# Optimization experiments

Hardware: AMD Instinct MI355X
Metric: run time of the kernel (lower is better)

The kernel has to match this reference:

```python
import jax, jax.numpy as jnp
import numpy as np

HID = 4096; H = 32; KVH = 8; D = 128
B = 4; Q = 256; KV = 2048; HIST = KV - Q
BS = 64; NB = KV // BS; NBLOCKS = 160
WINDOW = 1024; THETA = 10000.0


def _rope(x, pos):
    # x: [T, heads, D], pos: [T] absolute positions
    half = D // 2
    inv = 1.0 / (THETA ** (jnp.arange(half, dtype=jnp.float32) / half))
    f = pos.astype(jnp.float32)[:, None] * inv[None, :]          # [T, D/2]
    cos = jnp.concatenate([jnp.cos(f), jnp.cos(f)], -1)[:, None, :]
    sin = jnp.concatenate([jnp.sin(f), jnp.sin(f)], -1)[:, None, :]
    x1, x2 = jnp.split(x, 2, axis=-1)
    return x * cos + jnp.concatenate([-x2, x1], -1) * sin


def setup_inputs() -> dict:
    key = jax.random.key(0)
    ks = jax.random.split(key, 7)
    T = B * Q
    return dict(
        hidden_states=jax.random.normal(ks[0], (T, HID), jnp.float32),
        wq=jax.random.normal(ks[1], (HID, H * D), jnp.float32) * 0.02,
        wk=jax.random.normal(ks[2], (HID, KVH * D), jnp.float32) * 0.02,
        wv=jax.random.normal(ks[3], (HID, KVH * D), jnp.float32) * 0.02,
        wo=jax.random.normal(ks[4], (H * D, HID), jnp.float32) * 0.02,
        k_cache=jax.random.normal(ks[5], (NBLOCKS, BS, KVH, D), jnp.float32),
        v_cache=jax.random.normal(ks[6], (NBLOCKS, BS, KVH, D), jnp.float32),
        # each sequence appends Q new tokens at positions [HIST, KV)
        position_ids=jnp.tile(HIST + jnp.arange(Q, dtype=jnp.int32), B),
        q_start_loc=jnp.arange(B, dtype=jnp.int32) * Q,
        q_seq_length=jnp.full((B,), Q, jnp.int32),
        kv_seq_length=jnp.full((B,), KV, jnp.int32),
        block_offsets=jnp.arange(B * NB, dtype=jnp.int32).reshape(B, NB),
    )


def reference(hidden_states, wq, wk, wv, wo, k_cache, v_cache,
              position_ids, q_start_loc, q_seq_length, kv_seq_length,
              block_offsets):
    # qkv proj (no bias, Mistral)
    q = (hidden_states @ wq).reshape(-1, H, D)    # [T, H, D]
    k = (hidden_states @ wk).reshape(-1, KVH, D)  # [T, KVH, D]
    v = (hidden_states @ wv).reshape(-1, KVH, D)
    # rotary embedding on q, k with per-token absolute positions
    q = _rope(q, position_ids)
    k = _rope(k, position_ids)
    # fill paged KV cache: token with in-sequence slot s of sequence b goes to
    # block block_offsets[b, s // BS], offset s % BS
    b_idx = jnp.repeat(jnp.arange(B), Q)
    blk = block_offsets[b_idx, position_ids // BS]
    off = position_ids % BS
    k_cache = k_cache.at[blk, off].set(k)
    v_cache = v_cache.at[blk, off].set(v)
    # paged attention: gather each sequence's blocks from the cache
    k_all = k_cache[block_offsets].reshape(B, KV, KVH, D)
    v_all = v_cache[block_offsets].reshape(B, KV, KVH, D)
    G = H // KVH  # GQA group size
    qb = q.reshape(B, Q, KVH, G, D)
    scores = jnp.einsum('bqhgd,bkhd->bhgqk', qb, k_all) / jnp.sqrt(jnp.float32(D))
    # causal + sliding-window mask on absolute positions
    qpos = HIST + jnp.arange(Q)
    kpos = jnp.arange(KV)
    valid = (kpos[None, :] <= qpos[:, None]) & (kpos[None, :] > qpos[:, None] - WINDOW)
    scores = jnp.where(valid[None, None, None], scores, -jnp.inf)
    p = jax.nn.softmax(scores, axis=-1)
    o = jnp.einsum('bhgqk,bkhd->bqhgd', p, v_all).reshape(B * Q, H * D)
    return o @ wo
```

## Files before the change

kernel.cpp:

```cpp
#include <hip/hip_runtime.h>

#define BSZ  4
#define QL   256
#define KVL  2048
#define HIST 1792
#define WIN  1024
#define NH   32
#define NKVH 8
#define DH   128
#define HID  4096
#define SCALE 0.088388347648318447f
#define MFIX  8.0f

typedef __bf16 bf16x8 __attribute__((ext_vector_type(8)));
typedef float  fx4    __attribute__((ext_vector_type(4)));
typedef unsigned short us4 __attribute__((ext_vector_type(4)));
typedef unsigned short us8 __attribute__((ext_vector_type(8)));

__device__ __forceinline__ unsigned short f2bf(float x) {
    unsigned u = __float_as_uint(x);
    u += 0x7FFFu + ((u >> 16) & 1u);
    return (unsigned short)(u >> 16);
}
__device__ __forceinline__ float bf2f(unsigned short h) {
    return __uint_as_float(((unsigned)h) << 16);
}
__device__ __forceinline__ fx4 mfma16(bf16x8 a, bf16x8 b, fx4 c) {
    return __builtin_amdgcn_mfma_f32_16x16x32_bf16(a, b, c, 0, 0, 0);
}
__device__ __forceinline__ bf16x8 ldb16(const unsigned short* p) {
    return *reinterpret_cast<const bf16x8*>(p);
}

typedef __attribute__((address_space(1))) const void gv_t;
typedef __attribute__((address_space(3))) void lv_t;
__device__ __forceinline__ void gl16(const void* g, void* l) {
    __builtin_amdgcn_global_load_lds((gv_t*)g, (lv_t*)l, 16, 0, 0);
}

__device__ __forceinline__ void gemm_body(
    const unsigned short* __restrict__ A, const unsigned short* __restrict__ B,
    float* __restrict__ C0, float* __restrict__ Cz, size_t czstride,
    int lda, int ldc, int ksteps, int klast, int nx, int ny, int nz)
{
    constexpr int TILE = 128 * 32;
    __shared__ __align__(16) unsigned short lds[3 * 2 * TILE];

    const int per = gridDim.x >> 3;
    const int t = (blockIdx.x & 7) * per + (blockIdx.x >> 3);
    const int bx = t % nx;
    const int by = (t / nx) % ny;
    const int bz = t / (nx * ny);

    const int row0 = bx * 128;
    const int col0 = by * 128;
    const int kbase = bz * ksteps * 32;
    const int nks = (bz == nz - 1) ? klast : ksteps;
    float* Cm = (bz == 0) ? C0 : (Cz + (size_t)(bz - 1) * czstride);

    const int tid  = threadIdx.x;
    const int lane = tid & 63;
    const int w    = tid >> 6;
    const int wr   = w >> 1, wc = w & 1;
    const int l16  = lane & 15;
    const int lg   = lane >> 4;
    const int r_in = lane >> 2;
    const int c8   = (lane & 3) * 8;

    fx4 acc[4][4] = {};

    auto STAGE = [&](int bufi, int kp) {
        unsigned short* Lb = lds + bufi * (2 * TILE);
#pragma unroll
        for (int i = 0; i < 2; ++i) {
            const int r = w * 32 + i * 16 + r_in;
            const int ldsb = (w * 2 + i) * 512;
            gl16(A + (size_t)(row0 + r) * lda + kp + c8, Lb + ldsb);
            const int cr = col0 + r;
            const size_t baddr = ((size_t)(cr >> 6) * 64 + (kp >> 6)) * 4096
                               + (cr & 63) * 64 + (kp & 63) + c8;
            gl16(B + baddr, Lb + TILE + ldsb);
        }
    };

    STAGE(0, kbase);
    STAGE(1, kbase + 32);
    for (int ks = 0; ks < nks; ++ks) {
        if (ks + 2 < nks) {
            STAGE((ks + 2) % 3, kbase + (ks + 2) * 32);
            asm volatile("s_waitcnt vmcnt(8)" ::: "memory");
        } else if (ks + 1 < nks) {
            asm volatile("s_waitcnt vmcnt(4)" ::: "memory");
        } else {
            asm volatile("s_waitcnt vmcnt(0)" ::: "memory");
        }
        __builtin_amdgcn_s_barrier();
        __builtin_amdgcn_sched_barrier(0);

        const unsigned short* Lb = lds + (ks % 3) * (2 * TILE);
        const unsigned short* AhT = Lb;
        const unsigned short* BhT = Lb + TILE;

        bf16x8 af[4], bfv[4];
#pragma unroll
        for (int f = 0; f < 4; ++f) {
            af[f]  = ldb16(AhT + (wr * 64 + f * 16 + l16) * 32 + lg * 8);
            bfv[f] = ldb16(BhT + (wc * 64 + f * 16 + l16) * 32 + lg * 8);
        }
        __builtin_amdgcn_s_setprio(1);
#pragma unroll
        for (int fr = 0; fr < 4; ++fr)
#pragma unroll
            for (int fc = 0; fc < 4; ++fc)
                acc[fr][fc] = mfma16(af[fr], bfv[fc], acc[fr][fc]);
        __builtin_amdgcn_s_setprio(0);
        __builtin_amdgcn_sched_barrier(0);
        __builtin_amdgcn_s_barrier();
    }
#pragma unroll
    for (int fr = 0; fr < 4; ++fr)
#pragma unroll
        for (int fc = 0; fc < 4; ++fc) {
            const size_t rbase = (size_t)(row0 + wr * 64 + fr * 16 + lg * 4);
            const int col = col0 + wc * 64 + fc * 16 + l16;
#pragma unroll
            for (int r = 0; r < 4; ++r)
                Cm[(rbase + r) * ldc + col] = acc[fr][fc][r];
        }
}

__global__ __launch_bounds__(256) void qkv_gemm_kernel(
    const unsigned short* __restrict__ A, const unsigned short* __restrict__ B,
    float* __restrict__ C0, float* __restrict__ Cz, size_t czstride,
    int lda, int ldc, int ksteps, int klast, int nx, int ny, int nz)
{
    gemm_body(A, B, C0, Cz, czstride, lda, ldc, ksteps, klast, nx, ny, nz);
}

__global__ __launch_bounds__(256) void oproj_gemm_kernel(
    const unsigned short* __restrict__ A, const unsigned short* __restrict__ B,
    float* __restrict__ C0, float* __restrict__ Cz, size_t czstride,
    int lda, int ldc, int ksteps, int klast, int nx, int ny, int nz)
{
    gemm_body(A, B, C0, Cz, czstride, lda, ldc, ksteps, klast, nx, ny, nz);
}

__device__ __forceinline__ void transpose_tile(
    const float* __restrict__ w, unsigned short* __restrict__ hi, int N,
    int n0, int k0)
{
    __shared__ __align__(16) float shf[64][64];
    const int tid = threadIdx.x;
    const int rr = tid >> 4;
    const int cc = (tid & 15) * 4;
#pragma unroll
    for (int p = 0; p < 4; ++p) {
        const int kl = p * 16 + rr;
        fx4 v = *reinterpret_cast<const fx4*>(w + (size_t)(k0 + kl) * N + n0 + cc);
#pragma unroll
        for (int j = 0; j < 4; ++j) {
            const int n = cc + j;
            shf[n][kl ^ (n & 28)] = v[j];
        }
    }
    __syncthreads();
    unsigned short* ob = hi + (((size_t)(n0 >> 6)) * 64 + (k0 >> 6)) * 4096;
#pragma unroll
    for (int s = 0; s < 2; ++s) {
        const int c = s * 256 + tid;
        const int n = c >> 3;
        const int k8 = (c & 7) * 8;
        const int sw = n & 28;
        const int b0 = (k8 ^ (sw & 24)) | (sw & 4);
        fx4 v0 = *reinterpret_cast<const fx4*>(&shf[n][b0]);
        fx4 v1 = *reinterpret_cast<const fx4*>(&shf[n][b0 ^ 4]);
        us8 o;
#pragma unroll
        for (int j = 0; j < 4; ++j) {
            o[j]     = f2bf(v0[j]);
            o[4 + j] = f2bf(v1[j]);
        }
        *reinterpret_cast<us8*>(ob + c * 8) = o;
    }
}

__global__ __launch_bounds__(256) void prep_kernel(
    const float* __restrict__ wq, const float* __restrict__ wk,
    const float* __restrict__ wv, const float* __restrict__ wo,
    const float* __restrict__ hs,
    unsigned short* __restrict__ wqkvT, unsigned short* __restrict__ woTh,
    unsigned short* __restrict__ hsb, float* __restrict__ tab)
{
    const int r = blockIdx.x;
    const int tid = threadIdx.x;
    if (r < 4096) {
        transpose_tile(wq, wqkvT, 4096, (r & 63) * 64, (r >> 6) * 64);
    } else if (r < 5120) {
        const int r2 = r - 4096;
        transpose_tile(wk, wqkvT + (size_t)4096 * 4096, 1024,
                       (r2 & 15) * 64, (r2 >> 4) * 64);
    } else if (r < 6144) {
        const int r2 = r - 5120;
        transpose_tile(wv, wqkvT + (size_t)5120 * 4096, 1024,
                       (r2 & 15) * 64, (r2 >> 4) * 64);
    } else if (r < 10240) {
        const int r2 = r - 6144;
        transpose_tile(wo, woTh, 4096, (r2 & 63) * 64, (r2 >> 6) * 64);
    } else if (r < 12288) {
        const int r2 = r - 10240;
        int i = r2 * 256 + tid;
#pragma unroll
        for (int rep = 0; rep < 2; ++rep) {
            fx4 v = reinterpret_cast<const fx4*>(hs)[i];
            us4 o;
#pragma unroll
            for (int j = 0; j < 4; ++j) o[j] = f2bf(v[j]);
            reinterpret_cast<us4*>(hsb)[i] = o;
            i += 524288;
        }
    } else {
        const int r2 = r - 12288;
        const int qi = r2 * 4 + (tid >> 6);
        const int jr = tid & 63;
        const float inv = powf(10000.f, -(float)jr * (1.f / 64.f));
        const float f = (float)(HIST + qi) * inv;
        float s, c;
        sincosf(f, &s, &c);
        tab[(qi * 64 + jr) * 2]     = c;
        tab[(qi * 64 + jr) * 2 + 1] = s;
    }
}

__global__ __launch_bounds__(256) void rope_q_kernel(
    const float* __restrict__ qkv0, const float* __restrict__ qkv1,
    const int* __restrict__ pos_ids, const float* __restrict__ tab,
    unsigned short* __restrict__ qb)
{
    const int t = blockIdx.x;
    const int b = t >> 8;
    const int qi = t & 255;
    const int pi = pos_ids[t] - HIST;
    const int tid = threadIdx.x;
    const int h = tid >> 3;
    const int d0 = (tid & 7) * 8;
    const float* q0 = qkv0 + (size_t)t * 6144 + h * DH;
    const float* q1 = qkv1 + (size_t)t * 6144 + h * DH;
    float xl[8], xh[8];
    *reinterpret_cast<fx4*>(&xl[0]) = *reinterpret_cast<const fx4*>(q0 + d0)
                                    + *reinterpret_cast<const fx4*>(q1 + d0);
    *reinterpret_cast<fx4*>(&xl[4]) = *reinterpret_cast<const fx4*>(q0 + d0 + 4)
                                    + *reinterpret_cast<const fx4*>(q1 + d0 + 4);
    *reinterpret_cast<fx4*>(&xh[0]) = *reinterpret_cast<const fx4*>(q0 + d0 + 64)
                                    + *reinterpret_cast<const fx4*>(q1 + d0 + 64);
    *reinterpret_cast<fx4*>(&xh[4]) = *reinterpret_cast<const fx4*>(q0 + d0 + 68)
                                    + *reinterpret_cast<const fx4*>(q1 + d0 + 68);
    us8 outl, outh;
#pragma unroll
    for (int i = 0; i < 8; ++i) {
        const int jr = d0 + i;
        const float c = tab[(pi * 64 + jr) * 2];
        const float s = tab[(pi * 64 + jr) * 2 + 1];
        outl[i] = f2bf(xl[i] * c - xh[i] * s);
        outh[i] = f2bf(xh[i] * c + xl[i] * s);
    }
    unsigned short* dst = qb + (((size_t)b * NH + h) * QL + qi) * DH;
    *reinterpret_cast<us8*>(dst + d0)      = outl;
    *reinterpret_cast<us8*>(dst + d0 + 64) = outh;
}

__global__ __launch_bounds__(256) void gather_kv_kernel(
    const float* __restrict__ qkv0, const float* __restrict__ qkv1,
    const float* __restrict__ k_cache, const float* __restrict__ v_cache,
    const int* __restrict__ block_offsets, const float* __restrict__ tab,
    unsigned short* __restrict__ k_all, unsigned short* __restrict__ vT)
{
    __shared__ unsigned short vls[32][136];
    const int bid = blockIdx.x;
    const int xcd = bid & 7;
    const int i = bid >> 3;
    const int g = ((i & 31) << 3) | xcd;
    const int kh = i >> 5;
    const int b  = g >> 6;
    const int ck = g & 63;
    const int kv0 = ck * 32;
    const int tid = threadIdx.x;
    const int tok = tid >> 3;
    const int sl  = tid & 7;
    const int kvpos = kv0 + tok;
    const bool is_old = (kvpos < HIST);

    float x[16];
    float v[16];
    if (is_old) {
        const int blk = block_offsets[b * 32 + (kvpos >> 6)];
        const size_t base = (((size_t)blk * 64 + (kvpos & 63)) * NKVH + kh) * DH + sl * 4;
        const float* sk = k_cache + base;
        const float* sv = v_cache + base;
#pragma unroll
        for (int j = 0; j < 4; ++j) {
            *reinterpret_cast<fx4*>(&x[j * 4]) = *reinterpret_cast<const fx4*>(sk + j * 32);
            *reinterpret_cast<fx4*>(&v[j * 4]) = *reinterpret_cast<const fx4*>(sv + j * 32);
        }
    } else {
        const int t = b * QL + (kvpos - HIST);
        const int pi = kvpos - HIST;
        const size_t tb = (size_t)t * 6144 + kh * DH + sl * 4;
        const float* k0p = qkv0 + tb + 4096;
        const float* k1p = qkv1 + tb + 4096;
        const float* v0p = qkv0 + tb + 5120;
        const float* v1p = qkv1 + tb + 5120;
#pragma unroll
        for (int j = 0; j < 4; ++j) {
            *reinterpret_cast<fx4*>(&x[j * 4]) =
                *reinterpret_cast<const fx4*>(k0p + j * 32) +
                *reinterpret_cast<const fx4*>(k1p + j * 32);
            *reinterpret_cast<fx4*>(&v[j * 4]) =
                *reinterpret_cast<const fx4*>(v0p + j * 32) +
                *reinterpret_cast<const fx4*>(v1p + j * 32);
        }
#pragma unroll
        for (int j = 0; j < 2; ++j) {
            const int jr0 = sl * 4 + j * 32;
            fx4 cs0 = *reinterpret_cast<const fx4*>(tab + ((size_t)pi * 64 + jr0) * 2);
            fx4 cs1 = *reinterpret_cast<const fx4*>(tab + ((size_t)pi * 64 + jr0) * 2 + 4);
            const float c[4] = {cs0[0], cs0[2], cs1[0], cs1[2]};
            const float s[4] = {cs0[1], cs0[3], cs1[1], cs1[3]};
#pragma unroll
            for (int e = 0; e < 4; ++e) {
                const float lo = x[j * 4 + e], hi = x[(j + 2) * 4 + e];
                x[j * 4 + e]       = lo * c[e] - hi * s[e];
                x[(j + 2) * 4 + e] = hi * c[e] + lo * s[e];
            }
        }
    }
    {
        const size_t tbase = (((size_t)b * NKVH + kh) * KVL + kv0) * DH;
#pragma unroll
        for (int j = 0; j < 4; ++j) {
            const int d = sl * 4 + j * 32;
            const int dc = d >> 3;
            us4 pk;
#pragma unroll
            for (int e = 0; e < 4; ++e) pk[e] = f2bf(x[j * 4 + e]);
            *reinterpret_cast<us4*>(k_all + tbase + ((dc * 32 + tok) << 3) + (d & 7)) = pk;
        }
    }
#pragma unroll
    for (int j = 0; j < 4; ++j) {
        us4 pv;
#pragma unroll
        for (int e = 0; e < 4; ++e) pv[e] = f2bf(v[j * 4 + e]);
        *reinterpret_cast<us4*>(&vls[tok][sl * 4 + j * 32]) = pv;
    }
    __syncthreads();
    const int dr = tid >> 1;
    const int half = tid & 1;
    unsigned short* vtile = vT + (((size_t)b * NKVH + kh) * 64 + ck) * 4096;
#pragma unroll
    for (int i2 = 0; i2 < 16; i2 += 8) {
        const int kvc = half * 2 + (i2 >> 3);
        us8 pk;
#pragma unroll
        for (int j = 0; j < 8; ++j) pk[j] = vls[half * 16 + i2 + j][dr];
        *reinterpret_cast<us8*>(vtile + kvc * 1024 + dr * 8) = pk;
    }
}

__global__ __launch_bounds__(512) void attn_kernel(
    const unsigned short* __restrict__ qb,
    const unsigned short* __restrict__ kall,
    const unsigned short* __restrict__ vT,
    unsigned short* __restrict__ ohi)
{
    __shared__ __align__(16) unsigned short ldskv[4 * 8192];
    __shared__ __align__(16) unsigned short plds[8][16][88];

    const int bid = blockIdx.x;
    const int xcd = bid & 7, slot = bid >> 3;
    const int pair = xcd * 4 + (slot >> 3);
    const int within = slot & 7;
    const int kh = pair >> 2, b = pair & 3;
    const int qt = within & 3, p = within >> 2;

    const int tid = threadIdx.x;
    const int lane = tid & 63;
    const int w = tid >> 6;
    const int h = kh * 4 + p * 2 + (w >> 2);
    const int ww = w & 3;
    const int l16 = lane & 15;
    const int lg = lane >> 4;
    const int qrow0 = qt * 64 + ww * 16;
    const int qabs0 = HIST + qrow0;

    const unsigned short* qptr =
        qb + (((size_t)b * NH + h) * QL + qrow0 + l16) * DH + lg * 8;
    bf16x8 qf[4];
#pragma unroll
    for (int ds = 0; ds < 4; ++ds) qf[ds] = ldb16(qptr + ds * 32);

    fx4 oacc[8];
#pragma unroll
    for (int f = 0; f < 8; ++f) oacc[f] = (fx4){0.f, 0.f, 0.f, 0.f};
    float lsum[4] = {0.f, 0.f, 0.f, 0.f};

    const unsigned short* kbase = kall + ((size_t)b * NKVH + kh) * (KVL * DH);
    const unsigned short* vbase = vT + ((size_t)b * NKVH + kh) * (KVL * DH);

    const int kv_lo = ((HIST + qt * 64) - (WIN - 1)) & ~31;

    auto STAGE = [&](int bufi, int kv0) {
        unsigned short* kl = ldskv + bufi * 8192;
        const unsigned short* kg = kbase + (size_t)kv0 * DH;
        const unsigned short* vg = vbase + (size_t)(kv0 >> 5) * 4096;
        const int ci = w * 64 + lane;
        gl16(kg + ci * 8, kl + ci * 8);
        gl16(vg + ci * 8, kl + 4096 + ci * 8);
    };

    auto QK = [&](const unsigned short* kl, fx4& s0, fx4& s1) {
#pragma unroll
        for (int ds = 0; ds < 4; ++ds) {
            bf16x8 kf0 = ldb16(kl + ((ds * 4 + lg) * 32 + l16) * 8);
            bf16x8 kf1 = ldb16(kl + ((ds * 4 + lg) * 32 + 16 + l16) * 8);
            s0 = mfma16(qf[ds], kf0, s0);
            s1 = mfma16(qf[ds], kf1, s1);
        }
    };

    auto SM = [&](int kv0, fx4& s0, fx4& s1, int pc) {
        float p0v[4], p1v[4];
        const bool interior = (kv0 >= qabs0 + 16 - WIN) && (kv0 + 31 <= qabs0);
        if (interior) {
#pragma unroll
            for (int r = 0; r < 4; ++r) {
                p0v[r] = __expf(fmaf(s0[r], SCALE, -MFIX));
                p1v[r] = __expf(fmaf(s1[r], SCALE, -MFIX));
            }
        } else {
            const int kvp0 = kv0 + l16, kvp1 = kvp0 + 16;
#pragma unroll
            for (int r = 0; r < 4; ++r) {
                const int qpos = qabs0 + lg * 4 + r;
                const float e0 = __expf(fmaf(s0[r], SCALE, -MFIX));
                const float e1 = __expf(fmaf(s1[r], SCALE, -MFIX));
                p0v[r] = (kvp0 <= qpos && kvp0 > qpos - WIN) ? e0 : 0.f;
                p1v[r] = (kvp1 <= qpos && kvp1 > qpos - WIN) ? e1 : 0.f;
            }
        }
#pragma unroll
        for (int r = 0; r < 4; ++r) {
            lsum[r] += p0v[r] + p1v[r];
            plds[w][lg * 4 + r][pc + l16] = f2bf(p0v[r]);
            plds[w][lg * 4 + r][pc + 16 + l16] = f2bf(p1v[r]);
        }
    };

    auto PV = [&](const unsigned short* vl, bf16x8 pa) {
#pragma unroll
        for (int f = 0; f < 8; ++f) {
            bf16x8 vf = ldb16(vl + lg * 1024 + (f * 16 + l16) * 8);
            oacc[f] = mfma16(pa, vf, oacc[f]);
        }
    };

    STAGE(0, kv_lo);
    STAGE(1, kv_lo + 32);

    for (int t = 0; t < 34; t += 2) {
        if (t + 2 < 34) {
            STAGE((t + 2) & 3, kv_lo + (t + 2) * 32);
            STAGE((t + 3) & 3, kv_lo + (t + 3) * 32);
            asm volatile("s_waitcnt vmcnt(4)" ::: "memory");
        } else {
            asm volatile("s_waitcnt vmcnt(0)" ::: "memory");
        }
        __builtin_amdgcn_s_barrier();
        __builtin_amdgcn_sched_barrier(0);

        const unsigned short* kl0 = ldskv + (t & 3) * 8192;
        const unsigned short* kl1 = ldskv + ((t + 1) & 3) * 8192;

        fx4 sA0 = (fx4){0.f, 0.f, 0.f, 0.f}, sA1 = (fx4){0.f, 0.f, 0.f, 0.f};
        fx4 sB0 = (fx4){0.f, 0.f, 0.f, 0.f}, sB1 = (fx4){0.f, 0.f, 0.f, 0.f};
        __builtin_amdgcn_s_setprio(1);
        QK(kl0, sA0, sA1);
        QK(kl1, sB0, sB1);
        __builtin_amdgcn_s_setprio(0);

        SM(kv_lo + t * 32, sA0, sA1, 0);
        SM(kv_lo + (t + 1) * 32, sB0, sB1, 40);

        asm volatile("s_waitcnt lgkmcnt(0)" ::: "memory");
        __builtin_amdgcn_sched_barrier(0);
        bf16x8 pa0 = ldb16(&plds[w][l16][0 + lg * 8]);
        bf16x8 pa1 = ldb16(&plds[w][l16][40 + lg * 8]);
        __builtin_amdgcn_s_setprio(1);
        PV(kl0 + 4096, pa0);
        PV(kl1 + 4096, pa1);
        __builtin_amdgcn_s_setprio(0);
        __builtin_amdgcn_sched_barrier(0);
        __builtin_amdgcn_s_barrier();
    }
#pragma unroll
    for (int r = 0; r < 4; ++r) {
#pragma unroll
        for (int off = 1; off < 16; off <<= 1)
            lsum[r] += __shfl_xor(lsum[r], off);
    }
    float rl[4];
#pragma unroll
    for (int r = 0; r < 4; ++r) rl[r] = 1.f / lsum[r];
    const size_t obase = ((size_t)b * QL + qrow0 + lg * 4) * (NH * DH) + h * DH;
#pragma unroll
    for (int f = 0; f < 8; ++f)
#pragma unroll
        for (int r = 0; r < 4; ++r)
            ohi[obase + (size_t)r * (NH * DH) + f * 16 + l16] = f2bf(oacc[f][r] * rl[r]);
}

__global__ __launch_bounds__(256) void reduce_out_kernel(
    float* __restrict__ out, const float* __restrict__ parts)
{
    const int n4 = (1024 * 4096) / 4;
    int i = blockIdx.x * blockDim.x + threadIdx.x;
    for (; i < n4; i += gridDim.x * blockDim.x) {
        fx4 v = reinterpret_cast<fx4*>(out)[i] + reinterpret_cast<const fx4*>(parts)[i];
        reinterpret_cast<fx4*>(out)[i] = v;
    }
}

extern "C" void kernel_launch(void* const* d_in, const int* in_sizes, int n_in,
                              void* d_out, int out_size, void* d_ws, size_t ws_size,
                              hipStream_t stream)
{
    const float* hs = (const float*)d_in[0];
    const float* wq = (const float*)d_in[1];
    const float* wk = (const float*)d_in[2];
    const float* wv = (const float*)d_in[3];
    const float* wo = (const float*)d_in[4];
    const float* kc = (const float*)d_in[5];
    const float* vc = (const float*)d_in[6];
    const int* pos  = (const int*)d_in[7];
    const int* boff = (const int*)d_in[11];
    float* out = (float*)d_out;

    char* ws = (char*)d_ws;
    unsigned short* woTh  = (unsigned short*)(ws + 0);
    unsigned short* wqkvT = (unsigned short*)(ws + 67108864);
    unsigned short* kall  = (unsigned short*)(ws + 67108864);
    unsigned short* vTp   = (unsigned short*)(ws + 83886080);
    unsigned short* ohi   = (unsigned short*)(ws + 100663296);
    float* qkvb           = (float*)(ws + 117440512);
    float* oparts         = (float*)(ws + 117440512);
    unsigned short* hsb   = (unsigned short*)(ws + 167772160);
    unsigned short* qbb   = (unsigned short*)(ws + 167772160);
    float* tab            = (float*)(ws + 176160768);

    prep_kernel<<<12352, 256, 0, stream>>>(wq, wk, wv, wo, hs, wqkvT, woTh, hsb, tab);

    qkv_gemm_kernel<<<768, 256, 0, stream>>>(
        hsb, wqkvT,
        qkvb, qkvb + (size_t)1024 * 6144, (size_t)1024 * 6144,
        4096, 6144, 64, 64, 8, 48, 2);

    rope_q_kernel<<<1024, 256, 0, stream>>>(qkvb, qkvb + 6291456, pos, tab, qbb);
    gather_kv_kernel<<<2048, 256, 0, stream>>>(qkvb, qkvb + 6291456, kc, vc, boff, tab, kall, vTp);
    attn_kernel<<<256, 512, 0, stream>>>(qbb, kall, vTp, ohi);

    oproj_gemm_kernel<<<512, 256, 0, stream>>>(
        ohi, woTh,
        out, oparts, (size_t)1024 * 4096,
        4096, 4096, 64, 64, 8, 32, 2);
    reduce_out_kernel<<<2048, 256, 0, stream>>>(out, oparts);
}
```

Before: 232.9 us.

## Fuse wo transpose into the QKV GEMM launch to overlap with compute

The wo weight transpose and bf16 conversion moves out of the prep kernel and into extra blocks of the QKV GEMM launch. Each of these 2048 blocks handles two tiles and reuses the GEMM's shared-memory buffer. The aim is to overlap this memory-bound transpose with the compute-bound GEMM rather than run it serially in the prep kernel. GEMM parameters become hardcoded and the block index is passed in explicitly. The transpose blocks are dispatched first, so the real overlap may be limited to the boundary between the two kinds of blocks.

```diff
diff --git a/kernel.cpp b/kernel.cpp
--- a/kernel.cpp
+++ b/kernel.cpp
@@ -38,16 +38,54 @@
     __builtin_amdgcn_global_load_lds((gv_t*)g, (lv_t*)l, 16, 0, 0);
 }
 
+__device__ __forceinline__ void transpose_tile(
+    const float* __restrict__ w, unsigned short* __restrict__ hi, int N,
+    int n0, int k0, float* shf )
+{
+    const int tid = threadIdx.x & 255;
+    const int rr = tid >> 4;
+    const int cc = (tid & 15) * 4;
+#pragma unroll
+    for (int p = 0; p < 4; ++p) {
+        const int kl = p * 16 + rr;
+        fx4 v = *reinterpret_cast<const fx4*>(w + (size_t)(k0 + kl) * N + n0 + cc);
+#pragma unroll
+        for (int j = 0; j < 4; ++j) {
+            const int n = cc + j;
+            shf[n * 64 + (kl ^ (n & 28))] = v[j];
+        }
+    }
+    __syncthreads();
+    unsigned short* ob = hi + (((size_t)(n0 >> 6)) * 64 + (k0 >> 6)) * 4096;
+#pragma unroll
+    for (int s = 0; s < 2; ++s) {
+        const int c = s * 256 + tid;
+        const int n = c >> 3;
+        const int k8 = (c & 7) * 8;
+        const int sw = n & 28;
+        const int b0 = (k8 ^ (sw & 24)) | (sw & 4);
+        fx4 v0 = *reinterpret_cast<const fx4*>(&shf[n * 64 + b0]);
+        fx4 v1 = *reinterpret_cast<const fx4*>(&shf[n * 64 + (b0 ^ 4)]);
+        us8 o;
+#pragma unroll
+        for (int j = 0; j < 4; ++j) {
+            o[j]     = f2bf(v0[j]);
+            o[4 + j] = f2bf(v1[j]);
+        }
+        *reinterpret_cast<us8*>(ob + c * 8) = o;
+    }
+}
+
 __device__ __forceinline__ void gemm_body(
     const unsigned short* __restrict__ A, const unsigned short* __restrict__ B,
     float* __restrict__ C0, float* __restrict__ Cz, size_t czstride,
-    int lda, int ldc, int ksteps, int klast, int nx, int ny, int nz)
+    int lda, int ldc, int ksteps, int klast, int nx, int ny, int nz,
+    int bid, int nblocks, unsigned short* lds)
 {
     constexpr int TILE = 128 * 32;
-    __shared__ __align__(16) unsigned short lds[3 * 2 * TILE];
-
-    const int per = gridDim.x >> 3;
-    const int t = (blockIdx.x & 7) * per + (blockIdx.x >> 3);
+
+    const int per = nblocks >> 3;
+    const int t = (bid & 7) * per + (bid >> 3);
     const int bx = t % nx;
     const int by = (t / nx) % ny;
     const int bz = t / (nx * ny);
@@ -132,82 +170,53 @@
 __global__ __launch_bounds__(256) void qkv_gemm_kernel(
     const unsigned short* __restrict__ A, const unsigned short* __restrict__ B,
     float* __restrict__ C0, float* __restrict__ Cz, size_t czstride,
-    int lda, int ldc, int ksteps, int klast, int nx, int ny, int nz)
-{
-    gemm_body(A, B, C0, Cz, czstride, lda, ldc, ksteps, klast, nx, ny, nz);
+    const float* __restrict__ wo, unsigned short* __restrict__ woTh)
+{
+    __shared__ __align__(16) unsigned short lds[3 * 2 * 128 * 32];
+    const int bid = blockIdx.x;
+    if (bid < 2048) {
+        transpose_tile(wo, woTh, 4096, (bid & 63) * 64, (bid >> 6) * 64,
+                       reinterpret_cast<float*>(lds));
+        __syncthreads();
+        const int t2 = bid + 2048;
+        transpose_tile(wo, woTh, 4096, (t2 & 63) * 64, (t2 >> 6) * 64,
+                       reinterpret_cast<float*>(lds));
+    } else {
+        gemm_body(A, B, C0, Cz, czstride, 4096, 6144, 64, 64, 8, 48, 2,
+                  bid - 2048, 768, lds);
+    }
 }
 
 __global__ __launch_bounds__(256) void oproj_gemm_kernel(
     const unsigned short* __restrict__ A, const unsigned short* __restrict__ B,
-    float* __restrict__ C0, float* __restrict__ Cz, size_t czstride,
-    int lda, int ldc, int ksteps, int klast, int nx, int ny, int nz)
-{
-    gemm_body(A, B, C0, Cz, czstride, lda, ldc, ksteps, klast, nx, ny, nz);
-}
-
-__device__ __forceinline__ void transpose_tile(
-    const float* __restrict__ w, unsigned short* __restrict__ hi, int N,
-    int n0, int k0)
-{
-    __shared__ __align__(16) float shf[64][64];
-    const int tid = threadIdx.x;
-    const int rr = tid >> 4;
-    const int cc = (tid & 15) * 4;
-#pragma unroll
-    for (int p = 0; p < 4; ++p) {
-        const int kl = p * 16 + rr;
-        fx4 v = *reinterpret_cast<const fx4*>(w + (size_t)(k0 + kl) * N + n0 + cc);
-#pragma unroll
-        for (int j = 0; j < 4; ++j) {
-            const int n = cc + j;
-            shf[n][kl ^ (n & 28)] = v[j];
-        }
-    }
-    __syncthreads();
-    unsigned short* ob = hi + (((size_t)(n0 >> 6)) * 64 + (k0 >> 6)) * 4096;
-#pragma unroll
-    for (int s = 0; s < 2; ++s) {
-        const int c = s * 256 + tid;
-        const int n = c >> 3;
-        const int k8 = (c & 7) * 8;
-        const int sw = n & 28;
-        const int b0 = (k8 ^ (sw & 24)) | (sw & 4);
-        fx4 v0 = *reinterpret_cast<const fx4*>(&shf[n][b0]);
-        fx4 v1 = *reinterpret_cast<const fx4*>(&shf[n][b0 ^ 4]);
-        us8 o;
-#pragma unroll
-        for (int j = 0; j < 4; ++j) {
-            o[j]     = f2bf(v0[j]);
-            o[4 + j] = f2bf(v1[j]);
-        }
-        *reinterpret_cast<us8*>(ob + c * 8) = o;
-    }
+    float* __restrict__ C0, float* __restrict__ Cz, size_t czstride)
+{
+    __shared__ __align__(16) unsigned short lds[3 * 2 * 128 * 32];
+    gemm_body(A, B, C0, Cz, czstride, 4096, 4096, 64, 64, 8, 32, 2,
+              blockIdx.x, 512, lds);
 }
 
 __global__ __launch_bounds__(256) void prep_kernel(
     const float* __restrict__ wq, const float* __restrict__ wk,
-    const float* __restrict__ wv, const float* __restrict__ wo,
-    const float* __restrict__ hs,
-    unsigned short* __restrict__ wqkvT, unsigned short* __restrict__ woTh,
+    const float* __restrict__ wv, const float* __restrict__ hs,
+    unsigned short* __restrict__ wqkvT,
     unsigned short* __restrict__ hsb, float* __restrict__ tab)
 {
+    __shared__ __align__(16) float shf[64 * 64];
     const int r = blockIdx.x;
     const int tid = threadIdx.x;
     if (r < 4096) {
-        transpose_tile(wq, wqkvT, 4096, (r & 63) * 64, (r >> 6) * 64);
+        transpose_tile(wq, wqkvT, 4096, (r & 63) * 64, (r >> 6) * 64, shf);
     } else if (r < 5120) {
         const int r2 = r - 4096;
         transpose_tile(wk, wqkvT + (size_t)4096 * 4096, 1024,
-                       (r2 & 15) * 64, (r2 >> 4) * 64);
+                       (r2 & 15) * 64, (r2 >> 4) * 64, shf);
     } else if (r < 6144) {
         const int r2 = r - 5120;
         transpose_tile(wv, wqkvT + (size_t)5120 * 4096, 1024,
-                       (r2 & 15) * 64, (r2 >> 4) * 64);
-    } else if (r < 10240) {
+                       (r2 & 15) * 64, (r2 >> 4) * 64, shf);
+    } else if (r < 8192) {
         const int r2 = r - 6144;
-        transpose_tile(wo, woTh, 4096, (r2 & 63) * 64, (r2 >> 6) * 64);
-    } else if (r < 12288) {
-        const int r2 = r - 10240;
         int i = r2 * 256 + tid;
 #pragma unroll
         for (int rep = 0; rep < 2; ++rep) {
@@ -219,7 +228,7 @@
             i += 524288;
         }
     } else {
-        const int r2 = r - 12288;
+        const int r2 = r - 8192;
         const int qi = r2 * 4 + (tid >> 6);
         const int jr = tid & 63;
         const float inv = powf(10000.f, -(float)jr * (1.f / 64.f));
@@ -556,12 +565,12 @@
     unsigned short* qbb   = (unsigned short*)(ws + 167772160);
     float* tab            = (float*)(ws + 176160768);
 
-    prep_kernel<<<12352, 256, 0, stream>>>(wq, wk, wv, wo, hs, wqkvT, woTh, hsb, tab);
-
-    qkv_gemm_kernel<<<768, 256, 0, stream>>>(
+    prep_kernel<<<8256, 256, 0, stream>>>(wq, wk, wv, hs, wqkvT, hsb, tab);
+
+    qkv_gemm_kernel<<<2816, 256, 0, stream>>>(
         hsb, wqkvT,
         qkvb, qkvb + (size_t)1024 * 6144, (size_t)1024 * 6144,
-        4096, 6144, 64, 64, 8, 48, 2);
+        wo, woTh);
 
     rope_q_kernel<<<1024, 256, 0, stream>>>(qkvb, qkvb + 6291456, pos, tab, qbb);
     gather_kv_kernel<<<2048, 256, 0, stream>>>(qkvb, qkvb + 6291456, kc, vc, boff, tab, kall, vTp);
@@ -569,7 +578,6 @@
 
     oproj_gemm_kernel<<<512, 256, 0, stream>>>(
         ohi, woTh,
-        out, oparts, (size_t)1024 * 4096,
-        4096, 4096, 64, 64, 8, 32, 2);
+        out, oparts, (size_t)1024 * 4096);
     reduce_out_kernel<<<2048, 256, 0, stream>>>(out, oparts);
 }
```

Measured after the change: 230.4 us. No clear change (-1.1%).
